# Optimization experiments

Measured on AMD Instinct MI355X. Metric: run time of the kernel, lower is better.

Reference implementation:

```python
import jax, jax.numpy as jnp
import numpy as np

TOP_K = 8


def setup_inputs() -> dict:
    key = jax.random.key(0)
    ks = jax.random.split(key, 7)
    B, D, E = 65536, 1024, 64
    return {
        "x": jax.random.normal(ks[0], (B, D), dtype=jnp.float32),
        "Wg": jax.random.normal(ks[1], (E, D), dtype=jnp.float32) * 0.02,
        "bg": jax.random.normal(ks[2], (E,), dtype=jnp.float32) * 0.02,
        "Wn": jax.random.normal(ks[3], (E, D), dtype=jnp.float32) * 0.02,
        "bn": jax.random.normal(ks[4], (E,), dtype=jnp.float32) * 0.02,
        "We": jax.random.normal(ks[5], (E, D), dtype=jnp.float32) * 0.02,
        "noise": jax.random.normal(ks[6], (B, E), dtype=jnp.float32),
    }


def reference(x, Wg, bg, Wn, bn, We, noise):
    # Router (faithful to original: top-k is taken on noise_logits,
    # and noisy_logits is computed but does not affect the output).
    logits = x @ Wg.T + bg                      # [B, E]
    noise_logits = x @ Wn.T + bn                # [B, E]
    noisy_logits = logits + noise * jax.nn.softplus(noise_logits)  # unused downstream
    del noisy_logits

    top_vals, top_idx = jax.lax.top_k(noise_logits, TOP_K)  # [B, K]
    B, E = noise_logits.shape
    neg_inf = jnp.array(-jnp.inf, dtype=x.dtype)
    sparse_logits = jnp.full((B, E), neg_inf, dtype=x.dtype)
    sparse_logits = sparse_logits.at[jnp.arange(B)[:, None], top_idx].set(top_vals)
    routing_weights = jax.nn.softmax(sparse_logits, axis=-1)  # [B, E]

    # All experts are Linear(d, 1, bias=False): stack into one GEMM.
    expert_out = x @ We.T                        # [B, E]
    final_out = jnp.sum(expert_out * routing_weights, axis=-1, keepdims=True)  # [B, 1]
    return final_out
```

## Files before the change

kernel.cpp:

```cpp
#include <hip/hip_runtime.h>

#define DDIM 1024
#define NEXP 64
#define TOPK 8
#define BK 32
#define ROWS 64
#define NTILE (DDIM / BK)
#define TAU 2e-3f

typedef __attribute__((ext_vector_type(8))) short short8;
typedef __attribute__((ext_vector_type(4))) float f32x4;

static __device__ __forceinline__ unsigned int f2u(float f) { return __builtin_bit_cast(unsigned int, f); }
static __device__ __forceinline__ float u2f(unsigned int u) { return __builtin_bit_cast(float, u); }

static __device__ __forceinline__ unsigned short bf_hi_rne(float x) {
    unsigned int u = f2u(x);
    return (unsigned short)((u + (0x7FFFu + ((u >> 16) & 1u))) >> 16);
}

static __device__ __forceinline__ void split2(float x, unsigned short& h, unsigned short& l) {
    unsigned int u = f2u(x);
    unsigned int uh = (u + (0x7FFFu + ((u >> 16) & 1u))) & 0xFFFF0000u;
    h = (unsigned short)(uh >> 16);
    float rem = x - u2f(uh);
    l = (unsigned short)(f2u(rem) >> 16);
}

__global__ __launch_bounds__(256) void conv_w_kernel(
    const float* __restrict__ Wn, const float* __restrict__ We,
    unsigned short* __restrict__ wn_hi, unsigned short* __restrict__ wn_lo,
    unsigned short* __restrict__ we_hi)
{
    int i = blockIdx.x * 256 + threadIdx.x;
    unsigned short h, l;
    split2(Wn[i], h, l);
    wn_hi[i] = h;
    wn_lo[i] = l;
    we_hi[i] = bf_hi_rne(We[i]);
}

template <int PRE>
__global__ __launch_bounds__(256, 4) void moe_kernel(
    const float* __restrict__ x, const float* __restrict__ Wn,
    const float* __restrict__ bn, const float* __restrict__ We,
    const unsigned short* __restrict__ wn_hi, const unsigned short* __restrict__ wn_lo,
    const unsigned short* __restrict__ we_hi, float* __restrict__ out)
{
    __shared__ __align__(16) char smem[40960];

    const int tid = threadIdx.x;
    const int wid = tid >> 6;
    const int lane = tid & 63;
    const int fr = lane & 15;
    const int fq = lane >> 4;
    const int blockRow = blockIdx.x * ROWS;

    const int srow = tid >> 2, sg = tid & 3;
    const int swz = (srow * 64 + sg * 16) ^ ((srow & 7) << 4);
    const float* xsrc = x + (size_t)(blockRow + srow) * DDIM + sg * 8;

    f32x4 sx0, sx1;
    short8 sw0, sw1, sw2;
    f32x4 sn0, sn1, se0, se1;

    auto stage_load = [&](int t) {
        const int k0 = t * BK;
        sx0 = *(const f32x4*)(xsrc + k0);
        sx1 = *(const f32x4*)(xsrc + k0 + 4);
        if constexpr (PRE) {
            const int woff = srow * DDIM + k0 + sg * 8;
            sw0 = *(const short8*)(wn_hi + woff);
            sw1 = *(const short8*)(wn_lo + woff);
            sw2 = *(const short8*)(we_hi + woff);
        } else {
            const float* np = Wn + (size_t)srow * DDIM + k0 + sg * 8;
            const float* ep = We + (size_t)srow * DDIM + k0 + sg * 8;
            sn0 = ((const f32x4*)np)[0]; sn1 = ((const f32x4*)np)[1];
            se0 = ((const f32x4*)ep)[0]; se1 = ((const f32x4*)ep)[1];
        }
    };

    auto stage_write = [&](int b) {
        short8 xh, xl;
#pragma unroll
        for (int i = 0; i < 4; i++) { unsigned short h, l; split2(sx0[i], h, l); xh[i] = (short)h; xl[i] = (short)l; }
#pragma unroll
        for (int i = 0; i < 4; i++) { unsigned short h, l; split2(sx1[i], h, l); xh[i + 4] = (short)h; xl[i + 4] = (short)l; }
        char* xb = smem + b * 8192 + swz;
        *(short8*)(xb) = xh;
        *(short8*)(xb + 4096) = xl;
        char* wb = smem + 16384 + b * 12288 + swz;
        if constexpr (PRE) {
            *(short8*)(wb) = sw0;
            *(short8*)(wb + 4096) = sw1;
            *(short8*)(wb + 8192) = sw2;
        } else {
            short8 nh, nl, eh8;
#pragma unroll
            for (int i = 0; i < 4; i++) { unsigned short h, l; split2(sn0[i], h, l); nh[i] = (short)h; nl[i] = (short)l; }
#pragma unroll
            for (int i = 0; i < 4; i++) { unsigned short h, l; split2(sn1[i], h, l); nh[i + 4] = (short)h; nl[i + 4] = (short)l; }
#pragma unroll
            for (int i = 0; i < 4; i++) eh8[i] = (short)bf_hi_rne(se0[i]);
#pragma unroll
            for (int i = 0; i < 4; i++) eh8[i + 4] = (short)bf_hi_rne(se1[i]);
            *(short8*)(wb) = nh;
            *(short8*)(wb + 4096) = nl;
            *(short8*)(wb + 8192) = eh8;
        }
    };

    f32x4 accN[4], accE[4];
#pragma unroll
    for (int rt = 0; rt < 4; rt++) { accN[rt] = f32x4{0.f,0.f,0.f,0.f}; accE[rt] = f32x4{0.f,0.f,0.f,0.f}; }

    const int ecol = wid * 16 + fr;
    const int woffr = (ecol * 64 + fq * 16) ^ ((ecol & 7) << 4);

    auto compute = [&](int b) {
        const char* xb = smem + b * 8192;
        const char* wb = smem + 16384 + b * 12288;
        short8 wh = *(const short8*)(wb + woffr);
        short8 wl = *(const short8*)(wb + 4096 + woffr);
        short8 eh = *(const short8*)(wb + 8192 + woffr);
#pragma unroll
        for (int rt = 0; rt < 4; rt++) {
            const int row = rt * 16 + fr;
            const int xoff = (row * 64 + fq * 16) ^ ((row & 7) << 4);
            short8 xh = *(const short8*)(xb + xoff);
            short8 xl = *(const short8*)(xb + 4096 + xoff);
            accN[rt] = __builtin_amdgcn_mfma_f32_16x16x32_bf16(xh, wh, accN[rt], 0, 0, 0);
            accN[rt] = __builtin_amdgcn_mfma_f32_16x16x32_bf16(xh, wl, accN[rt], 0, 0, 0);
            accN[rt] = __builtin_amdgcn_mfma_f32_16x16x32_bf16(xl, wh, accN[rt], 0, 0, 0);
            accE[rt] = __builtin_amdgcn_mfma_f32_16x16x32_bf16(xh, eh, accE[rt], 0, 0, 0);
        }
    };

    stage_load(0);
    stage_write(0);
    stage_load(1);
    asm volatile("s_waitcnt lgkmcnt(0)" ::: "memory");
    __builtin_amdgcn_s_barrier();
    asm volatile("" ::: "memory");

#pragma unroll 2
    for (int t = 0; t < NTILE; ++t) {
        compute(t & 1);
        if (t < NTILE - 1) {
            stage_write((t + 1) & 1);
            if (t + 2 < NTILE) stage_load(t + 2);
            asm volatile("s_waitcnt lgkmcnt(0)" ::: "memory");
            __builtin_amdgcn_s_barrier();
            asm volatile("" ::: "memory");
        }
    }
    __syncthreads();

    float* s_log = (float*)smem;
    float* s_exp = (float*)(smem + 16640);
    float* s_vb  = (float*)(smem + 33280);

    const float be = bn[ecol];
#pragma unroll
    for (int rt = 0; rt < 4; rt++) {
#pragma unroll
        for (int j = 0; j < 4; j++) {
            const int r = rt * 16 + fq * 4 + j;
            s_log[r * 65 + ecol] = accN[rt][j] + be;
            s_exp[r * 65 + ecol] = accE[rt][j];
        }
    }
    __syncthreads();

    if (wid == 0) {
        auto do_row = [&](int r, float& gapo, float& vbo) -> float {
            float selv[TOPK]; int seli[TOPK];
            unsigned long long chosen = 0ull;
#pragma unroll
            for (int t = 0; t < TOPK; t++) {
                float best = -3.0e38f; int bi = 0;
#pragma unroll 4
                for (int e = 0; e < NEXP; e++) {
                    float v = s_log[r * 65 + e];
                    if (!((chosen >> e) & 1ull) && v > best) { best = v; bi = e; }
                }
                selv[t] = best; seli[t] = bi; chosen |= (1ull << bi);
            }
            float v9 = -3.0e38f;
#pragma unroll 4
            for (int e = 0; e < NEXP; e++) {
                float v = s_log[r * 65 + e];
                if (!((chosen >> e) & 1ull) && v > v9) v9 = v;
            }
            gapo = selv[TOPK - 1] - v9;
            vbo = 0.5f * (selv[TOPK - 1] + v9);
            float m = selv[0], Z = 0.f, o = 0.f;
#pragma unroll
            for (int t = 0; t < TOPK; t++) {
                float w = __expf(selv[t] - m);
                Z += w;
                o += w * s_exp[r * 65 + seli[t]];
            }
            return o / Z;
        };

        float gap, vb;
        float res = do_row(lane, gap, vb);
        out[blockRow + lane] = res;
        s_vb[lane] = vb;
        const bool flagged = (gap < TAU);
        unsigned long long flg = __ballot(flagged);

        while (flg) {
            const int r = __builtin_ctzll(flg);
            flg &= flg - 1;
            const float vbr = s_vb[r];
            const float ve = s_log[r * 65 + lane];
            unsigned long long cand = __ballot(fabsf(ve - vbr) <= TAU);
            const f32x4* xq = (const f32x4*)(x + (size_t)(blockRow + r) * DDIM) + lane * 4;
            const f32x4 xv0 = xq[0], xv1 = xq[1], xv2 = xq[2], xv3 = xq[3];
            while (cand) {
                const int ce = __builtin_ctzll(cand);
                cand &= cand - 1;
                const f32x4* wq = (const f32x4*)(Wn + (size_t)ce * DDIM) + lane * 4;
                const f32x4 w0 = wq[0], w1 = wq[1], w2 = wq[2], w3 = wq[3];
                double s = 0.0;
#pragma unroll
                for (int i = 0; i < 4; i++) s = fma((double)xv0[i], (double)w0[i], s);
#pragma unroll
                for (int i = 0; i < 4; i++) s = fma((double)xv1[i], (double)w1[i], s);
#pragma unroll
                for (int i = 0; i < 4; i++) s = fma((double)xv2[i], (double)w2[i], s);
#pragma unroll
                for (int i = 0; i < 4; i++) s = fma((double)xv3[i], (double)w3[i], s);
#pragma unroll
                for (int off = 32; off > 0; off >>= 1) s += __shfl_xor(s, off);
                s += (double)bn[ce];
                if (lane == 0) s_log[r * 65 + ce] = (float)s;
            }
        }
        if (flagged) {
            float g2, v2;
            out[blockRow + lane] = do_row(lane, g2, v2);
        }
    }
}

extern "C" void kernel_launch(void* const* d_in, const int* in_sizes, int n_in,
                              void* d_out, int out_size, void* d_ws, size_t ws_size,
                              hipStream_t stream)
{
    const float* x  = (const float*)d_in[0];
    const float* Wn = (const float*)d_in[3];
    const float* bn = (const float*)d_in[4];
    const float* We = (const float*)d_in[5];
    float* out = (float*)d_out;

    const int B = in_sizes[0] / DDIM;
    const int grid = B / ROWS;

    const size_t need = (size_t)NEXP * DDIM * sizeof(unsigned short) * 3;
    if (d_ws != nullptr && ws_size >= need) {
        unsigned short* wn_hi = (unsigned short*)d_ws;
        unsigned short* wn_lo = wn_hi + NEXP * DDIM;
        unsigned short* we_hi = wn_lo + NEXP * DDIM;
        conv_w_kernel<<<(NEXP * DDIM) / 256, 256, 0, stream>>>(Wn, We, wn_hi, wn_lo, we_hi);
        moe_kernel<1><<<grid, 256, 0, stream>>>(x, Wn, bn, We, wn_hi, wn_lo, we_hi, out);
    } else {
        moe_kernel<0><<<grid, 256, 0, stream>>>(x, Wn, bn, We, nullptr, nullptr, nullptr, out);
    }
}
```

Baseline: 110.1 us.

## Drop x low-part split, stream pre-swizzled weights via LDS DMA, parallelize fixup

Drops the bf16 low part of x, so the noise GEMM uses 2 MFMAs per tile instead of 3 and x staging in LDS halves. It compensates with wider tie-detection thresholds that trigger exact FP64 recomputation of near-boundary logits. The weights are pre-split and pre-swizzled into the LDS tile layout, then copied with global_load_lds, which moves them from global memory straight into LDS without going through registers. The top-k and fixup stages now spread across all four waves instead of one. The looser precision depends on the fallback catching every top-k boundary flip, and the wider thresholds may send more rows down the slow FP64 path.

```diff
diff --git a/kernel.cpp b/kernel.cpp
--- a/kernel.cpp
+++ b/kernel.cpp
@@ -5,8 +5,9 @@
 #define TOPK 8
 #define BK 32
 #define ROWS 64
-#define NTILE (DDIM / BK)
-#define TAU 2e-3f
+#define NTILE 32
+#define TAUF 1.0e-2f
+#define TAUB 2.0e-2f
 
 typedef __attribute__((ext_vector_type(8))) short short8;
 typedef __attribute__((ext_vector_type(4))) float f32x4;
@@ -28,26 +29,38 @@
 }
 
 __global__ __launch_bounds__(256) void conv_w_kernel(
-    const float* __restrict__ Wn, const float* __restrict__ We,
-    unsigned short* __restrict__ wn_hi, unsigned short* __restrict__ wn_lo,
-    unsigned short* __restrict__ we_hi)
+    const float* __restrict__ Wn, const float* __restrict__ We, char* __restrict__ wsW)
 {
-    int i = blockIdx.x * 256 + threadIdx.x;
-    unsigned short h, l;
-    split2(Wn[i], h, l);
-    wn_hi[i] = h;
-    wn_lo[i] = l;
-    we_hi[i] = bf_hi_rne(We[i]);
+    int g = blockIdx.x * 256 + threadIdx.x;
+    int e = g >> 7, c128 = g & 127;
+    int k = c128 << 3;
+    int t = k >> 5, c = (k >> 3) & 3;
+    const float* np = Wn + (size_t)e * DDIM + k;
+    const float* ep = We + (size_t)e * DDIM + k;
+    f32x4 n0 = ((const f32x4*)np)[0], n1 = ((const f32x4*)np)[1];
+    f32x4 e0 = ((const f32x4*)ep)[0], e1 = ((const f32x4*)ep)[1];
+    short8 nh, nl, eh;
+#pragma unroll
+    for (int i = 0; i < 4; i++) { unsigned short h, l; split2(n0[i], h, l); nh[i] = (short)h; nl[i] = (short)l; }
+#pragma unroll
+    for (int i = 0; i < 4; i++) { unsigned short h, l; split2(n1[i], h, l); nh[i + 4] = (short)h; nl[i + 4] = (short)l; }
+#pragma unroll
+    for (int i = 0; i < 4; i++) eh[i] = (short)bf_hi_rne(e0[i]);
+#pragma unroll
+    for (int i = 0; i < 4; i++) eh[i + 4] = (short)bf_hi_rne(e1[i]);
+    size_t dst = (size_t)t * 12288 + (size_t)((e * 64 + c * 16) ^ ((e & 7) << 4));
+    *(short8*)(wsW + dst)        = nh;
+    *(short8*)(wsW + dst + 4096) = nl;
+    *(short8*)(wsW + dst + 8192) = eh;
 }
 
 template <int PRE>
 __global__ __launch_bounds__(256, 4) void moe_kernel(
     const float* __restrict__ x, const float* __restrict__ Wn,
     const float* __restrict__ bn, const float* __restrict__ We,
-    const unsigned short* __restrict__ wn_hi, const unsigned short* __restrict__ wn_lo,
-    const unsigned short* __restrict__ we_hi, float* __restrict__ out)
+    const char* __restrict__ wsW, float* __restrict__ out)
 {
-    __shared__ __align__(16) char smem[40960];
+    __shared__ __align__(16) char smem[33792];
 
     const int tid = threadIdx.x;
     const int wid = tid >> 6;
@@ -61,54 +74,52 @@
     const float* xsrc = x + (size_t)(blockRow + srow) * DDIM + sg * 8;
 
     f32x4 sx0, sx1;
-    short8 sw0, sw1, sw2;
     f32x4 sn0, sn1, se0, se1;
 
-    auto stage_load = [&](int t) {
-        const int k0 = t * BK;
-        sx0 = *(const f32x4*)(xsrc + k0);
-        sx1 = *(const f32x4*)(xsrc + k0 + 4);
-        if constexpr (PRE) {
-            const int woff = srow * DDIM + k0 + sg * 8;
-            sw0 = *(const short8*)(wn_hi + woff);
-            sw1 = *(const short8*)(wn_lo + woff);
-            sw2 = *(const short8*)(we_hi + woff);
-        } else {
-            const float* np = Wn + (size_t)srow * DDIM + k0 + sg * 8;
-            const float* ep = We + (size_t)srow * DDIM + k0 + sg * 8;
+    auto xload = [&](int t) {
+        const float* p = xsrc + t * BK;
+        sx0 = ((const f32x4*)p)[0];
+        sx1 = ((const f32x4*)p)[1];
+        if constexpr (!PRE) {
+            const float* np = Wn + (size_t)srow * DDIM + t * BK + sg * 8;
+            const float* ep = We + (size_t)srow * DDIM + t * BK + sg * 8;
             sn0 = ((const f32x4*)np)[0]; sn1 = ((const f32x4*)np)[1];
             se0 = ((const f32x4*)ep)[0]; se1 = ((const f32x4*)ep)[1];
         }
     };
 
     auto stage_write = [&](int b) {
-        short8 xh, xl;
-#pragma unroll
-        for (int i = 0; i < 4; i++) { unsigned short h, l; split2(sx0[i], h, l); xh[i] = (short)h; xl[i] = (short)l; }
-#pragma unroll
-        for (int i = 0; i < 4; i++) { unsigned short h, l; split2(sx1[i], h, l); xh[i + 4] = (short)h; xl[i + 4] = (short)l; }
-        char* xb = smem + b * 8192 + swz;
-        *(short8*)(xb) = xh;
-        *(short8*)(xb + 4096) = xl;
-        char* wb = smem + 16384 + b * 12288 + swz;
-        if constexpr (PRE) {
-            *(short8*)(wb) = sw0;
-            *(short8*)(wb + 4096) = sw1;
-            *(short8*)(wb + 8192) = sw2;
-        } else {
-            short8 nh, nl, eh8;
+        short8 xh;
+#pragma unroll
+        for (int i = 0; i < 4; i++) xh[i] = (short)bf_hi_rne(sx0[i]);
+#pragma unroll
+        for (int i = 0; i < 4; i++) xh[i + 4] = (short)bf_hi_rne(sx1[i]);
+        *(short8*)(smem + b * 4096 + swz) = xh;
+        if constexpr (!PRE) {
+            short8 nh, nl, eh;
 #pragma unroll
             for (int i = 0; i < 4; i++) { unsigned short h, l; split2(sn0[i], h, l); nh[i] = (short)h; nl[i] = (short)l; }
 #pragma unroll
             for (int i = 0; i < 4; i++) { unsigned short h, l; split2(sn1[i], h, l); nh[i + 4] = (short)h; nl[i + 4] = (short)l; }
 #pragma unroll
-            for (int i = 0; i < 4; i++) eh8[i] = (short)bf_hi_rne(se0[i]);
-#pragma unroll
-            for (int i = 0; i < 4; i++) eh8[i + 4] = (short)bf_hi_rne(se1[i]);
-            *(short8*)(wb) = nh;
+            for (int i = 0; i < 4; i++) eh[i] = (short)bf_hi_rne(se0[i]);
+#pragma unroll
+            for (int i = 0; i < 4; i++) eh[i + 4] = (short)bf_hi_rne(se1[i]);
+            char* wb = smem + 8192 + b * 12288 + swz;
+            *(short8*)(wb)        = nh;
             *(short8*)(wb + 4096) = nl;
-            *(short8*)(wb + 8192) = eh8;
-        }
+            *(short8*)(wb + 8192) = eh;
+        }
+    };
+
+    auto wdma = [&](int t, int b) {
+        const char* gs = wsW + (size_t)t * 12288 + wid * 1024 + lane * 16;
+        char* ls = smem + 8192 + b * 12288 + wid * 1024;
+#pragma unroll
+        for (int i = 0; i < 3; i++)
+            __builtin_amdgcn_global_load_lds(
+                (const __attribute__((address_space(1))) void*)(gs + i * 4096),
+                (__attribute__((address_space(3))) void*)(ls + i * 4096), 16, 0, 0);
     };
 
     f32x4 accN[4], accE[4];
@@ -119,8 +130,7 @@
     const int woffr = (ecol * 64 + fq * 16) ^ ((ecol & 7) << 4);
 
     auto compute = [&](int b) {
-        const char* xb = smem + b * 8192;
-        const char* wb = smem + 16384 + b * 12288;
+        const char* wb = smem + 8192 + b * 12288;
         short8 wh = *(const short8*)(wb + woffr);
         short8 wl = *(const short8*)(wb + 4096 + woffr);
         short8 eh = *(const short8*)(wb + 8192 + woffr);
@@ -128,29 +138,37 @@
         for (int rt = 0; rt < 4; rt++) {
             const int row = rt * 16 + fr;
             const int xoff = (row * 64 + fq * 16) ^ ((row & 7) << 4);
-            short8 xh = *(const short8*)(xb + xoff);
-            short8 xl = *(const short8*)(xb + 4096 + xoff);
+            short8 xh = *(const short8*)(smem + b * 4096 + xoff);
             accN[rt] = __builtin_amdgcn_mfma_f32_16x16x32_bf16(xh, wh, accN[rt], 0, 0, 0);
             accN[rt] = __builtin_amdgcn_mfma_f32_16x16x32_bf16(xh, wl, accN[rt], 0, 0, 0);
-            accN[rt] = __builtin_amdgcn_mfma_f32_16x16x32_bf16(xl, wh, accN[rt], 0, 0, 0);
             accE[rt] = __builtin_amdgcn_mfma_f32_16x16x32_bf16(xh, eh, accE[rt], 0, 0, 0);
         }
     };
 
-    stage_load(0);
+    xload(0);
+    if constexpr (PRE) wdma(0, 0);
     stage_write(0);
-    stage_load(1);
-    asm volatile("s_waitcnt lgkmcnt(0)" ::: "memory");
+    xload(1);
+    if constexpr (PRE) asm volatile("s_waitcnt vmcnt(2) lgkmcnt(0)" ::: "memory");
+    else               asm volatile("s_waitcnt lgkmcnt(0)" ::: "memory");
     __builtin_amdgcn_s_barrier();
     asm volatile("" ::: "memory");
 
-#pragma unroll 2
     for (int t = 0; t < NTILE; ++t) {
-        compute(t & 1);
-        if (t < NTILE - 1) {
-            stage_write((t + 1) & 1);
-            if (t + 2 < NTILE) stage_load(t + 2);
-            asm volatile("s_waitcnt lgkmcnt(0)" ::: "memory");
+        const int cur = t & 1, nxt = cur ^ 1;
+        if (t + 1 < NTILE) {
+            if constexpr (PRE) wdma(t + 1, nxt);
+            stage_write(nxt);
+            if (t + 2 < NTILE) xload(t + 2);
+        }
+        compute(cur);
+        if (t + 1 < NTILE) {
+            if constexpr (PRE) {
+                if (t + 2 < NTILE) asm volatile("s_waitcnt vmcnt(2) lgkmcnt(0)" ::: "memory");
+                else               asm volatile("s_waitcnt vmcnt(0) lgkmcnt(0)" ::: "memory");
+            } else {
+                asm volatile("s_waitcnt lgkmcnt(0)" ::: "memory");
+            }
             __builtin_amdgcn_s_barrier();
             asm volatile("" ::: "memory");
         }
@@ -159,7 +177,8 @@
 
     float* s_log = (float*)smem;
     float* s_exp = (float*)(smem + 16640);
-    float* s_vb  = (float*)(smem + 33280);
+    float* s_gap = (float*)(smem + 33280);
+    float* s_vb  = (float*)(smem + 33536);
 
     const float be = bn[ecol];
 #pragma unroll
@@ -173,76 +192,80 @@
     }
     __syncthreads();
 
-    if (wid == 0) {
-        auto do_row = [&](int r, float& gapo, float& vbo) -> float {
-            float selv[TOPK]; int seli[TOPK];
-            unsigned long long chosen = 0ull;
-#pragma unroll
-            for (int t = 0; t < TOPK; t++) {
-                float best = -3.0e38f; int bi = 0;
-#pragma unroll 4
-                for (int e = 0; e < NEXP; e++) {
-                    float v = s_log[r * 65 + e];
-                    if (!((chosen >> e) & 1ull) && v > best) { best = v; bi = e; }
-                }
-                selv[t] = best; seli[t] = bi; chosen |= (1ull << bi);
-            }
-            float v9 = -3.0e38f;
+    auto do_row = [&](int r, float& gapo, float& vbo) -> float {
+        float selv[TOPK]; int seli[TOPK];
+        unsigned long long chosen = 0ull;
+#pragma unroll
+        for (int t = 0; t < TOPK; t++) {
+            float best = -3.0e38f; int bi = 0;
 #pragma unroll 4
             for (int e = 0; e < NEXP; e++) {
                 float v = s_log[r * 65 + e];
-                if (!((chosen >> e) & 1ull) && v > v9) v9 = v;
+                if (!((chosen >> e) & 1ull) && v > best) { best = v; bi = e; }
             }
-            gapo = selv[TOPK - 1] - v9;
-            vbo = 0.5f * (selv[TOPK - 1] + v9);
-            float m = selv[0], Z = 0.f, o = 0.f;
-#pragma unroll
-            for (int t = 0; t < TOPK; t++) {
-                float w = __expf(selv[t] - m);
-                Z += w;
-                o += w * s_exp[r * 65 + seli[t]];
-            }
-            return o / Z;
-        };
-
+            selv[t] = best; seli[t] = bi; chosen |= (1ull << bi);
+        }
+        float v9 = -3.0e38f;
+#pragma unroll 4
+        for (int e = 0; e < NEXP; e++) {
+            float v = s_log[r * 65 + e];
+            if (!((chosen >> e) & 1ull) && v > v9) v9 = v;
+        }
+        gapo = selv[TOPK - 1] - v9;
+        vbo = 0.5f * (selv[TOPK - 1] + v9);
+        float m = selv[0], Z = 0.f, o = 0.f;
+#pragma unroll
+        for (int t = 0; t < TOPK; t++) {
+            float w = __expf(selv[t] - m);
+            Z += w;
+            o += w * s_exp[r * 65 + seli[t]];
+        }
+        return o / Z;
+    };
+
+    if (lane < 16) {
+        const int r = wid * 16 + lane;
         float gap, vb;
-        float res = do_row(lane, gap, vb);
-        out[blockRow + lane] = res;
-        s_vb[lane] = vb;
-        const bool flagged = (gap < TAU);
-        unsigned long long flg = __ballot(flagged);
-
-        while (flg) {
-            const int r = __builtin_ctzll(flg);
-            flg &= flg - 1;
-            const float vbr = s_vb[r];
-            const float ve = s_log[r * 65 + lane];
-            unsigned long long cand = __ballot(fabsf(ve - vbr) <= TAU);
-            const f32x4* xq = (const f32x4*)(x + (size_t)(blockRow + r) * DDIM) + lane * 4;
-            const f32x4 xv0 = xq[0], xv1 = xq[1], xv2 = xq[2], xv3 = xq[3];
-            while (cand) {
-                const int ce = __builtin_ctzll(cand);
-                cand &= cand - 1;
-                const f32x4* wq = (const f32x4*)(Wn + (size_t)ce * DDIM) + lane * 4;
-                const f32x4 w0 = wq[0], w1 = wq[1], w2 = wq[2], w3 = wq[3];
-                double s = 0.0;
-#pragma unroll
-                for (int i = 0; i < 4; i++) s = fma((double)xv0[i], (double)w0[i], s);
-#pragma unroll
-                for (int i = 0; i < 4; i++) s = fma((double)xv1[i], (double)w1[i], s);
-#pragma unroll
-                for (int i = 0; i < 4; i++) s = fma((double)xv2[i], (double)w2[i], s);
-#pragma unroll
-                for (int i = 0; i < 4; i++) s = fma((double)xv3[i], (double)w3[i], s);
-#pragma unroll
-                for (int off = 32; off > 0; off >>= 1) s += __shfl_xor(s, off);
-                s += (double)bn[ce];
-                if (lane == 0) s_log[r * 65 + ce] = (float)s;
-            }
-        }
-        if (flagged) {
+        float res = do_row(r, gap, vb);
+        out[blockRow + r] = res;
+        s_gap[r] = gap; s_vb[r] = vb;
+    }
+    __syncthreads();
+
+    for (int r = wid; r < ROWS; r += 4) {
+        if (!(s_gap[r] < TAUF)) continue;
+        const float vbr = s_vb[r];
+        const float ve = s_log[r * 65 + lane];
+        unsigned long long cand = __ballot(fabsf(ve - vbr) <= TAUB);
+        const f32x4* xq = (const f32x4*)(x + (size_t)(blockRow + r) * DDIM) + lane * 4;
+        const f32x4 xv0 = xq[0], xv1 = xq[1], xv2 = xq[2], xv3 = xq[3];
+        while (cand) {
+            const int ce = __builtin_ctzll(cand);
+            cand &= cand - 1;
+            const f32x4* wq = (const f32x4*)(Wn + (size_t)ce * DDIM) + lane * 4;
+            const f32x4 w0 = wq[0], w1 = wq[1], w2 = wq[2], w3 = wq[3];
+            double s = 0.0;
+#pragma unroll
+            for (int i = 0; i < 4; i++) s = fma((double)xv0[i], (double)w0[i], s);
+#pragma unroll
+            for (int i = 0; i < 4; i++) s = fma((double)xv1[i], (double)w1[i], s);
+#pragma unroll
+            for (int i = 0; i < 4; i++) s = fma((double)xv2[i], (double)w2[i], s);
+#pragma unroll
+            for (int i = 0; i < 4; i++) s = fma((double)xv3[i], (double)w3[i], s);
+#pragma unroll
+            for (int off = 32; off > 0; off >>= 1) s += __shfl_xor(s, off);
+            s += (double)bn[ce];
+            if (lane == 0) s_log[r * 65 + ce] = (float)s;
+        }
+    }
+    __syncthreads();
+
+    if (lane < 16) {
+        const int r = wid * 16 + lane;
+        if (s_gap[r] < TAUF) {
             float g2, v2;
-            out[blockRow + lane] = do_row(lane, g2, v2);
+            out[blockRow + r] = do_row(r, g2, v2);
         }
     }
 }
@@ -260,14 +283,11 @@
     const int B = in_sizes[0] / DDIM;
     const int grid = B / ROWS;
 
-    const size_t need = (size_t)NEXP * DDIM * sizeof(unsigned short) * 3;
+    const size_t need = (size_t)NTILE * 12288;
     if (d_ws != nullptr && ws_size >= need) {
-        unsigned short* wn_hi = (unsigned short*)d_ws;
-        unsigned short* wn_lo = wn_hi + NEXP * DDIM;
-        unsigned short* we_hi = wn_lo + NEXP * DDIM;
-        conv_w_kernel<<<(NEXP * DDIM) / 256, 256, 0, stream>>>(Wn, We, wn_hi, wn_lo, we_hi);
-        moe_kernel<1><<<grid, 256, 0, stream>>>(x, Wn, bn, We, wn_hi, wn_lo, we_hi, out);
+        conv_w_kernel<<<(NEXP * DDIM / 8) / 256, 256, 0, stream>>>(Wn, We, (char*)d_ws);
+        moe_kernel<1><<<grid, 256, 0, stream>>>(x, Wn, bn, We, (const char*)d_ws, out);
     } else {
-        moe_kernel<0><<<grid, 256, 0, stream>>>(x, Wn, bn, We, nullptr, nullptr, nullptr, out);
-    }
-}
+        moe_kernel<0><<<grid, 256, 0, stream>>>(x, Wn, bn, We, nullptr, out);
+    }
+}
```

New measurement: 135.4 us. +23.0%, slower.
